# Kernel optimization log

Measured on AMD Instinct MI355X. Metric: run time of the kernel, lower is better.

Reference implementation:

```python
import jax, jax.numpy as jnp
import numpy as np

VOCAB = 8; D = 256; H = 8; DH = 32; SEQ = 4096; N_LAYERS = 4; N_CLASS = 10
BUCKET = 64; N_HASHES = 2; N_BUCKETS = SEQ // BUCKET; B = 8


def setup_inputs() -> dict:
    key = jax.random.key(0)
    ks = iter(jax.random.split(key, 24))
    s = 0.02
    inp = {}
    inp['x'] = jax.random.randint(next(ks), (B, SEQ), 0, VOCAB)
    inp['emb'] = jax.random.normal(next(ks), (VOCAB, D)) * s
    inp['posenc'] = jax.random.normal(next(ks), (SEQ, D)) * s
    inp['ln1_g'] = jnp.ones((N_LAYERS, D)); inp['ln1_b'] = jnp.zeros((N_LAYERS, D))
    inp['Wqk'] = jax.random.normal(next(ks), (N_LAYERS, D, D)) * s
    inp['Wv'] = jax.random.normal(next(ks), (N_LAYERS, D, D)) * s
    inp['Wo'] = jax.random.normal(next(ks), (N_LAYERS, D, D)) * s
    inp['ln2_g'] = jnp.ones((N_LAYERS, D)); inp['ln2_b'] = jnp.zeros((N_LAYERS, D))
    inp['W1'] = jax.random.normal(next(ks), (N_LAYERS, D, 4 * D)) * s
    inp['b1'] = jnp.zeros((N_LAYERS, 4 * D))
    inp['W2'] = jax.random.normal(next(ks), (N_LAYERS, 4 * D, D)) * s
    inp['b2'] = jnp.zeros((N_LAYERS, D))
    inp['rot'] = jax.random.normal(next(ks), (N_LAYERS, N_HASHES, DH, N_BUCKETS // 2))
    inp['Wf'] = jax.random.normal(next(ks), (SEQ * D, N_CLASS)) * s
    inp['bf'] = jnp.zeros((N_CLASS,))
    return inp


def layer_norm(x, g, b):
    m = x.mean(-1, keepdims=True)
    v = ((x - m) ** 2).mean(-1, keepdims=True)
    return (x - m) * jax.lax.rsqrt(v + 1e-5) * g + b


def look_back(t):
    # concatenate each chunk with the previous chunk (wrap-around roll, as in lucidrains)
    return jnp.concatenate([t, jnp.roll(t, 1, axis=2)], axis=3)


def lsh_attention(x, Wqk, Wv, Wo, rot):
    b, s, _ = x.shape
    qk = (x @ Wqk).reshape(b, s, H, DH).transpose(0, 2, 1, 3)  # b h s dh (shared QK)
    v = (x @ Wv).reshape(b, s, H, DH).transpose(0, 2, 1, 3)
    # LSH hashing: random rotations, bucket = argmax over [r, -r]
    r = jnp.einsum('bhsd,ndr->bhnsr', qk, rot)
    buckets = jnp.argmax(jnp.concatenate([r, -r], axis=-1), axis=-1)  # b h n s
    buckets = buckets + jnp.arange(N_HASHES)[:, None] * N_BUCKETS
    buckets = buckets.reshape(b, H, N_HASHES * s)
    ticker = jnp.arange(N_HASHES * s) % s
    sticker = jnp.argsort(buckets * s + ticker, axis=-1)  # stable sort by (bucket, pos)
    undo = jnp.argsort(sticker, axis=-1)
    st = sticker % s  # original seq positions, bucket-sorted
    sqk = jnp.take_along_axis(qk, st[..., None], axis=2)
    sv = jnp.take_along_axis(v, st[..., None], axis=2)
    nch = N_HASHES * N_BUCKETS
    bq = sqk.reshape(b, H, nch, BUCKET, DH)
    bk = bq / jnp.maximum(jnp.linalg.norm(bq, axis=-1, keepdims=True), 1e-6)  # keys = l2-normed qk
    bv = sv.reshape(b, H, nch, BUCKET, DH)
    bk, bv = look_back(bk), look_back(bv)
    stq = st.reshape(b, H, nch, BUCKET)
    stk = look_back(stq)
    dots = jnp.einsum('bhcqd,bhckd->bhcqk', bq, bk) * (DH ** -0.5)
    dots = jnp.where(stq[..., :, None] < stk[..., None, :], -1e9, dots)   # causal
    dots = jnp.where(stq[..., :, None] == stk[..., None, :], -1e5, dots)  # self-mask
    lse = jax.nn.logsumexp(dots, axis=-1, keepdims=True)
    bo = jnp.einsum('bhcqk,bhckd->bhcqd', jnp.exp(dots - lse), bv)
    so = bo.reshape(b, H, N_HASHES * s, DH)
    slog = lse.reshape(b, H, N_HASHES * s)
    o = jnp.take_along_axis(so, undo[..., None], axis=2).reshape(b, H, N_HASHES, s, DH)
    lg = jnp.take_along_axis(slog, undo, axis=2).reshape(b, H, N_HASHES, s, 1)
    out = (o * jax.nn.softmax(lg, axis=2)).sum(axis=2)  # combine hash rounds by logits
    return out.transpose(0, 2, 1, 3).reshape(b, s, D) @ Wo


def reference(x, emb, posenc, ln1_g, ln1_b, Wqk, Wv, Wo, ln2_g, ln2_b, W1, b1, W2, b2, rot, Wf, bf):
    h = emb[x] + posenc[None]
    x1, x2 = h, h  # reversible two-stream (torch.cat([x, x]))
    for l in range(N_LAYERS):
        x1 = x1 + lsh_attention(layer_norm(x2, ln1_g[l], ln1_b[l]), Wqk[l], Wv[l], Wo[l], rot[l])
        ff_in = layer_norm(x1, ln2_g[l], ln2_b[l])
        x2 = x2 + jax.nn.gelu(ff_in @ W1[l] + b1[l]) @ W2[l] + b2[l]
    y = 0.5 * (x1 + x2)  # stack(chunk(2)).mean(0)
    return y.reshape(y.shape[0], -1) @ Wf + bf
```

## Files before the change

### kernel.cpp

```cpp
#include <hip/hip_runtime.h>
#include <hip/hip_bf16.h>
#include <math.h>

#define SEQ 4096
#define D 256
#define H 8
#define DH 32
#define B 8
#define NL 4
#define NH 2
#define NTOK (B*SEQ)

__global__ __launch_bounds__(256) void k_embed(const int* __restrict__ x,
    const float* __restrict__ emb, const float* __restrict__ pos,
    float* __restrict__ x1, float* __restrict__ x2) {
  int t = blockIdx.x; int d = threadIdx.x;
  int s = t & (SEQ - 1);
  int tok = x[t];
  float v = emb[tok * D + d] + pos[(size_t)s * D + d];
  x1[(size_t)t * D + d] = v;
  x2[(size_t)t * D + d] = v;
}

__global__ __launch_bounds__(256) void k_ln(const float* __restrict__ X,
    const float* __restrict__ g, const float* __restrict__ bta,
    float* __restrict__ Y) {
  int lane = threadIdx.x & 63, wv = threadIdx.x >> 6;
  int row = blockIdx.x * 4 + wv;
  const float* xr = X + (size_t)row * D;
  float v[4]; float s = 0.f;
  #pragma unroll
  for (int j = 0; j < 4; j++) { v[j] = xr[lane + 64 * j]; s += v[j]; }
  #pragma unroll
  for (int off = 32; off; off >>= 1) s += __shfl_xor(s, off);
  float m = s * (1.0f / D);
  float vs = 0.f;
  #pragma unroll
  for (int j = 0; j < 4; j++) { float d0 = v[j] - m; vs += d0 * d0; }
  #pragma unroll
  for (int off = 32; off; off >>= 1) vs += __shfl_xor(vs, off);
  float inv = rsqrtf(vs * (1.0f / D) + 1e-5f);
  float* yr = Y + (size_t)row * D;
  #pragma unroll
  for (int j = 0; j < 4; j++) {
    int d0 = lane + 64 * j;
    yr[d0] = (v[j] - m) * inv * g[d0] + bta[d0];
  }
}

__device__ __forceinline__ float gelu_f(float x) {
  float x3 = x * x * x;
  return 0.5f * x * (1.0f + tanhf(0.7978845608028654f * (x + 0.044715f * x3)));
}

template<int MODE>
__global__ __launch_bounds__(256) void k_gemm(const float* __restrict__ A,
    const float* __restrict__ Bm, float* __restrict__ C,
    const float* __restrict__ bias, int M, int N, int K,
    int lda, int ldb, int ldc) {
  __shared__ float As[16][68];
  __shared__ float Bs[16][68];
  int tid = threadIdx.x;
  int tx = tid & 15, ty = tid >> 4;
  int row0 = blockIdx.y * 64, col0 = blockIdx.x * 64;
  int arow = tid >> 2, ac4 = tid & 3;
  int brow = tid >> 4, bc4 = tid & 15;
  float acc[4][4] = {};
  for (int k0 = 0; k0 < K; k0 += 16) {
    float4 av = *(const float4*)(A + (size_t)(row0 + arow) * lda + k0 + ac4 * 4);
    float4 bv = *(const float4*)(Bm + (size_t)(k0 + brow) * ldb + col0 + bc4 * 4);
    __syncthreads();
    As[ac4 * 4 + 0][arow] = av.x;
    As[ac4 * 4 + 1][arow] = av.y;
    As[ac4 * 4 + 2][arow] = av.z;
    As[ac4 * 4 + 3][arow] = av.w;
    *(float4*)&Bs[brow][bc4 * 4] = bv;
    __syncthreads();
    #pragma unroll
    for (int kk = 0; kk < 16; ++kk) {
      float4 a = *(float4*)&As[kk][ty * 4];
      float4 b = *(float4*)&Bs[kk][tx * 4];
      float ar[4] = {a.x, a.y, a.z, a.w};
      float br[4] = {b.x, b.y, b.z, b.w};
      #pragma unroll
      for (int i = 0; i < 4; i++)
        #pragma unroll
        for (int j = 0; j < 4; j++)
          acc[i][j] = fmaf(ar[i], br[j], acc[i][j]);
    }
  }
  #pragma unroll
  for (int i = 0; i < 4; i++) {
    int gr = row0 + ty * 4 + i;
    #pragma unroll
    for (int j = 0; j < 4; j++) {
      int gc = col0 + tx * 4 + j;
      float vv = acc[i][j];
      if constexpr (MODE == 1) {
        int b0 = gr >> 12, s0 = gr & 4095, h0 = gc >> 5, d0 = gc & 31;
        C[((size_t)(b0 * H + h0) * SEQ + s0) * DH + d0] = vv;
      } else if constexpr (MODE == 2) {
        C[(size_t)gr * ldc + gc] = gelu_f(vv + bias[gc]);
      } else {
        float add = bias ? bias[gc] : 0.f;
        C[(size_t)gr * ldc + gc] += vv + add;
      }
    }
  }
}

__global__ __launch_bounds__(256) void k_hash(const float* __restrict__ qk,
    const float* __restrict__ rot, int* __restrict__ st) {
  __shared__ float rs[32][33];
  __shared__ int sb[SEQ];
  __shared__ int hist[64];
  __shared__ int start[64];
  int tid = threadIdx.x;
  int bh = blockIdx.x >> 1, n = blockIdx.x & 1;
  const float* rotn = rot + n * DH * 32;
  for (int i = tid; i < 1024; i += 256) rs[i >> 5][i & 31] = rotn[i];
  if (tid < 64) hist[tid] = 0;
  __syncthreads();
  const float* qkb = qk + (size_t)bh * SEQ * DH;
  for (int s = tid; s < SEQ; s += 256) {
    float q[32];
    const float* qr = qkb + (size_t)s * DH;
    #pragma unroll
    for (int d = 0; d < 32; d += 4) {
      float4 t4 = *(const float4*)(qr + d);
      q[d] = t4.x; q[d + 1] = t4.y; q[d + 2] = t4.z; q[d + 3] = t4.w;
    }
    float bp = -1e30f, bn = -1e30f; int bpi = 0, bni = 0;
    for (int j = 0; j < 32; j++) {
      float rv = 0.f;
      #pragma unroll
      for (int d = 0; d < 32; d++) rv = fmaf(q[d], rs[d][j], rv);
      if (rv > bp) { bp = rv; bpi = j; }
      if (-rv > bn) { bn = -rv; bni = j; }
    }
    sb[s] = (bp >= bn) ? bpi : (bni + 32);
  }
  __syncthreads();
  for (int s = tid; s < SEQ; s += 256) atomicAdd(&hist[sb[s]], 1);
  __syncthreads();
  if (tid == 0) {
    int acc = 0;
    for (int j = 0; j < 64; j++) { start[j] = acc; acc += hist[j]; }
  }
  __syncthreads();
  if (tid < 64) {
    int j = tid;
    int* outp = st + (size_t)blockIdx.x * SEQ;
    int pos = start[j];
    for (int p = 0; p < SEQ; p++) if (sb[p] == j) outp[pos++] = p;
  }
}

template<int NHALF>
__global__ __launch_bounds__(256) void k_attn(const float* __restrict__ qk,
    const float* __restrict__ v, const int* __restrict__ st,
    float* __restrict__ o_acc, float* __restrict__ lg) {
  __shared__ float qs[64][36];
  __shared__ float vs[128][36];
  __shared__ float dots[64][129];
  __shared__ float lse_s[64];
  __shared__ int stq[64];
  __shared__ int stk[128];
  int tid = threadIdx.x;
  int bh = blockIdx.x >> 6, cl = blockIdx.x & 63;
  int c = NHALF * 64 + cl;
  int pc = (c + 127) & 127, pn = pc >> 6;
  const int* stb = st + (size_t)bh * 2 * SEQ;
  if (tid < 64) {
    int q0 = stb[NHALF * SEQ + cl * 64 + tid];
    stq[tid] = q0; stk[tid] = q0;
  } else if (tid < 128) {
    int kk = tid - 64;
    stk[64 + kk] = stb[pn * SEQ + (pc & 63) * 64 + kk];
  }
  __syncthreads();
  const float* qkb = qk + (size_t)bh * SEQ * DH;
  const float* vb  = v  + (size_t)bh * SEQ * DH;
  for (int idx = tid; idx < 512; idx += 256) {
    int r = idx >> 3, j = idx & 7;
    *(float4*)&qs[r][j * 4] = *(const float4*)(qkb + (size_t)stq[r] * DH + j * 4);
  }
  for (int idx = tid; idx < 1024; idx += 256) {
    int r = idx >> 3, j = idx & 7;
    *(float4*)&vs[r][j * 4] = *(const float4*)(vb + (size_t)stk[r] * DH + j * 4);
  }
  int col = tid & 127;
  int rh = tid >> 7;
  float4 kf[8];
  int kpos = stk[col];
  {
    const float* kr = qkb + (size_t)kpos * DH;
    float nrm = 0.f;
    #pragma unroll
    for (int j = 0; j < 8; j++) {
      kf[j] = *(const float4*)(kr + j * 4);
      nrm += kf[j].x * kf[j].x + kf[j].y * kf[j].y + kf[j].z * kf[j].z + kf[j].w * kf[j].w;
    }
    float sc = 0.17677669529663687f / fmaxf(sqrtf(nrm), 1e-6f);
    #pragma unroll
    for (int j = 0; j < 8; j++) { kf[j].x *= sc; kf[j].y *= sc; kf[j].z *= sc; kf[j].w *= sc; }
  }
  __syncthreads();
  for (int r0 = 0; r0 < 32; ++r0) {
    int r = rh * 32 + r0;
    float dsum = 0.f;
    #pragma unroll
    for (int j = 0; j < 8; j++) {
      float4 qv = *(float4*)&qs[r][j * 4];
      dsum = fmaf(qv.x, kf[j].x, dsum);
      dsum = fmaf(qv.y, kf[j].y, dsum);
      dsum = fmaf(qv.z, kf[j].z, dsum);
      dsum = fmaf(qv.w, kf[j].w, dsum);
    }
    int sq = stq[r];
    float dd = dsum;
    if (sq == kpos) dd = -1e5f;
    else if (sq < kpos) dd = -1e9f;
    dots[r][col] = dd;
  }
  __syncthreads();
  int lane = tid & 63, wv = tid >> 6;
  for (int rr = 0; rr < 16; ++rr) {
    int r = wv * 16 + rr;
    float d0 = dots[r][lane], d1 = dots[r][lane + 64];
    float m = fmaxf(d0, d1);
    #pragma unroll
    for (int off = 32; off; off >>= 1) m = fmaxf(m, __shfl_xor(m, off));
    float e0 = expf(d0 - m), e1 = expf(d1 - m);
    float ssum = e0 + e1;
    #pragma unroll
    for (int off = 32; off; off >>= 1) ssum += __shfl_xor(ssum, off);
    float inv = 1.0f / ssum;
    dots[r][lane] = e0 * inv;
    dots[r][lane + 64] = e1 * inv;
    if (lane == 0) lse_s[r] = m + logf(ssum);
  }
  __syncthreads();
  int r = tid >> 2, dq = (tid & 3) << 3;
  float4 a0 = make_float4(0, 0, 0, 0), a1 = make_float4(0, 0, 0, 0);
  for (int cc = 0; cc < 128; ++cc) {
    float p = dots[r][cc];
    float4 v0 = *(float4*)&vs[cc][dq];
    float4 v1 = *(float4*)&vs[cc][dq + 4];
    a0.x = fmaf(p, v0.x, a0.x); a0.y = fmaf(p, v0.y, a0.y);
    a0.z = fmaf(p, v0.z, a0.z); a0.w = fmaf(p, v0.w, a0.w);
    a1.x = fmaf(p, v1.x, a1.x); a1.y = fmaf(p, v1.y, a1.y);
    a1.z = fmaf(p, v1.z, a1.z); a1.w = fmaf(p, v1.w, a1.w);
  }
  int pos = stq[r];
  int b0 = bh >> 3, h0 = bh & 7;
  float* orow = o_acc + ((size_t)b0 * SEQ + pos) * D + h0 * DH + dq;
  if constexpr (NHALF == 0) {
    *(float4*)orow = a0;
    *(float4*)(orow + 4) = a1;
  } else {
    float l0 = lg[(size_t)bh * SEQ + pos];
    float l1 = lse_s[r];
    float m = fmaxf(l0, l1);
    float w0 = expf(l0 - m), w1 = expf(l1 - m);
    float inv = 1.0f / (w0 + w1);
    float4 o0 = *(float4*)orow;
    float4 o1 = *(float4*)(orow + 4);
    o0.x = (w0 * o0.x + w1 * a0.x) * inv;
    o0.y = (w0 * o0.y + w1 * a0.y) * inv;
    o0.z = (w0 * o0.z + w1 * a0.z) * inv;
    o0.w = (w0 * o0.w + w1 * a0.w) * inv;
    o1.x = (w0 * o1.x + w1 * a1.x) * inv;
    o1.y = (w0 * o1.y + w1 * a1.y) * inv;
    o1.z = (w0 * o1.z + w1 * a1.z) * inv;
    o1.w = (w0 * o1.w + w1 * a1.w) * inv;
    *(float4*)orow = o0;
    *(float4*)(orow + 4) = o1;
  }
  if constexpr (NHALF == 0) {
    if (tid < 64) lg[(size_t)bh * SEQ + stq[tid]] = lse_s[tid];
  }
}

__global__ __launch_bounds__(128) void k_initout(const float* __restrict__ bf,
                                                 float* __restrict__ outp) {
  int i = threadIdx.x;
  if (i < 80) outp[i] = bf[i % 10];
}

__global__ __launch_bounds__(256) void k_cls(const float* __restrict__ x1,
    const float* __restrict__ x2, const float* __restrict__ Wf,
    float* __restrict__ outp) {
  __shared__ float wsum[4];
  int tid = threadIdx.x;
  size_t ib = (size_t)blockIdx.x * 1024 + tid * 4;
  int lane = tid & 63, wv = tid >> 6;
  for (int b0 = 0; b0 < B; ++b0) {
    const float* p1 = x1 + (size_t)b0 * (SEQ * D) + ib;
    const float* p2 = x2 + (size_t)b0 * (SEQ * D) + ib;
    float4 y1 = *(const float4*)p1;
    float4 y2 = *(const float4*)p2;
    float y[4] = {0.5f * (y1.x + y2.x), 0.5f * (y1.y + y2.y),
                  0.5f * (y1.z + y2.z), 0.5f * (y1.w + y2.w)};
    float acc[10] = {};
    #pragma unroll
    for (int t = 0; t < 4; ++t) {
      const float* wr = Wf + (ib + t) * 10;
      #pragma unroll
      for (int c0 = 0; c0 < 10; ++c0) acc[c0] = fmaf(y[t], wr[c0], acc[c0]);
    }
    #pragma unroll 1
    for (int c0 = 0; c0 < 10; ++c0) {
      float sv = acc[c0];
      #pragma unroll
      for (int off = 32; off; off >>= 1) sv += __shfl_xor(sv, off);
      if (lane == 0) wsum[wv] = sv;
      __syncthreads();
      if (tid == 0) atomicAdd(&outp[b0 * 10 + c0], wsum[0] + wsum[1] + wsum[2] + wsum[3]);
      __syncthreads();
    }
  }
}

extern "C" void kernel_launch(void* const* d_in, const int* in_sizes, int n_in,
                              void* d_out, int out_size, void* d_ws, size_t ws_size,
                              hipStream_t stream) {
  const int*   x    = (const int*)  d_in[0];
  const float* emb  = (const float*)d_in[1];
  const float* pos  = (const float*)d_in[2];
  const float* ln1g = (const float*)d_in[3];
  const float* ln1b = (const float*)d_in[4];
  const float* Wqk  = (const float*)d_in[5];
  const float* Wv   = (const float*)d_in[6];
  const float* Wo   = (const float*)d_in[7];
  const float* ln2g = (const float*)d_in[8];
  const float* ln2b = (const float*)d_in[9];
  const float* W1   = (const float*)d_in[10];
  const float* b1   = (const float*)d_in[11];
  const float* W2   = (const float*)d_in[12];
  const float* b2   = (const float*)d_in[13];
  const float* rot  = (const float*)d_in[14];
  const float* Wf   = (const float*)d_in[15];
  const float* bf   = (const float*)d_in[16];
  float* outp = (float*)d_out;

  const size_t SZ = (size_t)NTOK * D;
  float* x1  = (float*)d_ws;
  float* x2  = x1 + SZ;
  float* tln = x1 + 2 * SZ;
  float* och = tln;
  float* qk  = x1 + 3 * SZ;
  float* vv  = x1 + 4 * SZ;
  float* lg  = x1 + 5 * SZ;
  int*   st  = (int*)(lg + (size_t)B * H * SEQ);
  float* mid = qk;

  k_embed<<<NTOK, 256, 0, stream>>>(x, emb, pos, x1, x2);
  for (int l = 0; l < NL; ++l) {
    k_ln<<<NTOK / 4, 256, 0, stream>>>(x2, ln1g + l * D, ln1b + l * D, tln);
    k_gemm<1><<<dim3(D / 64, NTOK / 64), 256, 0, stream>>>(
        tln, Wqk + (size_t)l * D * D, qk, nullptr, NTOK, D, D, D, D, 0);
    k_gemm<1><<<dim3(D / 64, NTOK / 64), 256, 0, stream>>>(
        tln, Wv + (size_t)l * D * D, vv, nullptr, NTOK, D, D, D, D, 0);
    k_hash<<<B * H * NH, 256, 0, stream>>>(qk, rot + (size_t)l * NH * DH * 32, st);
    k_attn<0><<<B * H * 64, 256, 0, stream>>>(qk, vv, st, och, lg);
    k_attn<1><<<B * H * 64, 256, 0, stream>>>(qk, vv, st, och, lg);
    k_gemm<3><<<dim3(D / 64, NTOK / 64), 256, 0, stream>>>(
        och, Wo + (size_t)l * D * D, x1, nullptr, NTOK, D, D, D, D, D);
    k_ln<<<NTOK / 4, 256, 0, stream>>>(x1, ln2g + l * D, ln2b + l * D, tln);
    k_gemm<2><<<dim3(1024 / 64, NTOK / 64), 256, 0, stream>>>(
        tln, W1 + (size_t)l * D * 1024, mid, b1 + (size_t)l * 1024,
        NTOK, 1024, D, D, 1024, 1024);
    k_gemm<3><<<dim3(D / 64, NTOK / 64), 256, 0, stream>>>(
        mid, W2 + (size_t)l * 1024 * D, x2, b2 + (size_t)l * D,
        NTOK, D, 1024, 1024, D, D);
  }
  k_initout<<<1, 128, 0, stream>>>(bf, outp);
  k_cls<<<1024, 256, 0, stream>>>(x1, x2, Wf, outp);
}
```

Measured before the change: 6.396 ms.

## Use 128x128 register-blocked FP32 GEMM with prefetch and split FFN hidden dim

The GEMM moves from 64x64 tiles with 4x4 per-thread outputs to 128x128 tiles with 8x8 per-thread outputs. Global loads for the next K-slice are prefetched into registers while the current slice is computed, and results are written as float4 vectors. The FFN is split into two 512-wide halves, with W2 accumulating into x2 after each half, so the intermediate buffer is half the size. The classifier kernel keeps Wf in registers and reduces all 10 classes together, using one sync pair per batch instead of one per class. The cost is higher register pressure, which can lower occupancy, and fewer GEMM blocks (512 for the DxD GEMMs).

```diff
diff --git a/kernel.cpp b/kernel.cpp
--- a/kernel.cpp
+++ b/kernel.cpp
@@ -10,6 +10,11 @@
 #define NL 4
 #define NH 2
 #define NTOK (B*SEQ)
+
+__device__ __forceinline__ float gelu_f(float x) {
+  float x3 = x * x * x;
+  return 0.5f * x * (1.0f + tanhf(0.7978845608028654f * (x + 0.044715f * x3)));
+}
 
 __global__ __launch_bounds__(256) void k_embed(const int* __restrict__ x,
     const float* __restrict__ emb, const float* __restrict__ pos,
@@ -48,63 +53,82 @@
   }
 }
 
-__device__ __forceinline__ float gelu_f(float x) {
-  float x3 = x * x * x;
-  return 0.5f * x * (1.0f + tanhf(0.7978845608028654f * (x + 0.044715f * x3)));
-}
-
 template<int MODE>
-__global__ __launch_bounds__(256) void k_gemm(const float* __restrict__ A,
+__global__ __launch_bounds__(256) void k_gemm_f32(const float* __restrict__ A,
     const float* __restrict__ Bm, float* __restrict__ C,
-    const float* __restrict__ bias, int M, int N, int K,
-    int lda, int ldb, int ldc) {
-  __shared__ float As[16][68];
-  __shared__ float Bs[16][68];
-  int tid = threadIdx.x;
-  int tx = tid & 15, ty = tid >> 4;
-  int row0 = blockIdx.y * 64, col0 = blockIdx.x * 64;
-  int arow = tid >> 2, ac4 = tid & 3;
-  int brow = tid >> 4, bc4 = tid & 15;
-  float acc[4][4] = {};
+    const float* __restrict__ bias, int K, int lda, int ldb, int ldc, int N) {
+  __shared__ float As[16][132];
+  __shared__ float Bs[16][132];
+  int t = threadIdx.x;
+  int tx = t & 15, ty = t >> 4;
+  int row0 = blockIdx.y * 128, col0 = blockIdx.x * 128;
+  int ar = t >> 1, akq = (t & 1) * 8;
+  int bk = t >> 4, bcq = (t & 15) * 8;
+  const float* ap = A + (size_t)(row0 + ar) * lda + akq;
+  const float* bp = Bm + (size_t)bk * ldb + col0 + bcq;
+  float4 a0 = *(const float4*)(ap);
+  float4 a1 = *(const float4*)(ap + 4);
+  float4 b0 = *(const float4*)(bp);
+  float4 b1 = *(const float4*)(bp + 4);
+  float acc[8][8] = {};
   for (int k0 = 0; k0 < K; k0 += 16) {
-    float4 av = *(const float4*)(A + (size_t)(row0 + arow) * lda + k0 + ac4 * 4);
-    float4 bv = *(const float4*)(Bm + (size_t)(k0 + brow) * ldb + col0 + bc4 * 4);
     __syncthreads();
-    As[ac4 * 4 + 0][arow] = av.x;
-    As[ac4 * 4 + 1][arow] = av.y;
-    As[ac4 * 4 + 2][arow] = av.z;
-    As[ac4 * 4 + 3][arow] = av.w;
-    *(float4*)&Bs[brow][bc4 * 4] = bv;
+    As[akq + 0][ar] = a0.x; As[akq + 1][ar] = a0.y;
+    As[akq + 2][ar] = a0.z; As[akq + 3][ar] = a0.w;
+    As[akq + 4][ar] = a1.x; As[akq + 5][ar] = a1.y;
+    As[akq + 6][ar] = a1.z; As[akq + 7][ar] = a1.w;
+    *(float4*)&Bs[bk][bcq] = b0;
+    *(float4*)&Bs[bk][bcq + 4] = b1;
     __syncthreads();
+    if (k0 + 16 < K) {
+      a0 = *(const float4*)(ap + k0 + 16);
+      a1 = *(const float4*)(ap + k0 + 20);
+      const float* bpk = Bm + (size_t)(k0 + 16 + bk) * ldb + col0 + bcq;
+      b0 = *(const float4*)(bpk);
+      b1 = *(const float4*)(bpk + 4);
+    }
     #pragma unroll
     for (int kk = 0; kk < 16; ++kk) {
-      float4 a = *(float4*)&As[kk][ty * 4];
-      float4 b = *(float4*)&Bs[kk][tx * 4];
-      float ar[4] = {a.x, a.y, a.z, a.w};
-      float br[4] = {b.x, b.y, b.z, b.w};
-      #pragma unroll
-      for (int i = 0; i < 4; i++)
+      float a[8], b[8];
+      *(float4*)&a[0] = *(float4*)&As[kk][ty * 8];
+      *(float4*)&a[4] = *(float4*)&As[kk][ty * 8 + 4];
+      *(float4*)&b[0] = *(float4*)&Bs[kk][tx * 8];
+      *(float4*)&b[4] = *(float4*)&Bs[kk][tx * 8 + 4];
+      #pragma unroll
+      for (int i = 0; i < 8; i++)
         #pragma unroll
-        for (int j = 0; j < 4; j++)
-          acc[i][j] = fmaf(ar[i], br[j], acc[i][j]);
-    }
-  }
-  #pragma unroll
-  for (int i = 0; i < 4; i++) {
-    int gr = row0 + ty * 4 + i;
-    #pragma unroll
-    for (int j = 0; j < 4; j++) {
-      int gc = col0 + tx * 4 + j;
-      float vv = acc[i][j];
-      if constexpr (MODE == 1) {
-        int b0 = gr >> 12, s0 = gr & 4095, h0 = gc >> 5, d0 = gc & 31;
-        C[((size_t)(b0 * H + h0) * SEQ + s0) * DH + d0] = vv;
-      } else if constexpr (MODE == 2) {
-        C[(size_t)gr * ldc + gc] = gelu_f(vv + bias[gc]);
-      } else {
-        float add = bias ? bias[gc] : 0.f;
-        C[(size_t)gr * ldc + gc] += vv + add;
-      }
+        for (int j = 0; j < 8; j++)
+          acc[i][j] = fmaf(a[i], b[j], acc[i][j]);
+    }
+  }
+  #pragma unroll
+  for (int i = 0; i < 8; i++) {
+    int gr = row0 + ty * 8 + i;
+    int gc0 = col0 + tx * 8;
+    if constexpr (MODE == 0) {
+      int b0i = gr >> 12, s0 = gr & 4095, h0 = gc0 >> 5, d0 = gc0 & 31;
+      float* dst = C + ((size_t)(b0i * H + h0) * SEQ + s0) * DH + d0;
+      *(float4*)dst = *(float4*)&acc[i][0];
+      *(float4*)(dst + 4) = *(float4*)&acc[i][4];
+    } else if constexpr (MODE == 2) {
+      float* dst = C + (size_t)gr * ldc + gc0;
+      float o[8];
+      #pragma unroll
+      for (int j = 0; j < 8; j++) o[j] = gelu_f(acc[i][j] + bias[gc0 + j]);
+      *(float4*)dst = *(float4*)&o[0];
+      *(float4*)(dst + 4) = *(float4*)&o[4];
+    } else {
+      float* dst = C + (size_t)gr * ldc + gc0;
+      float4 c0 = *(float4*)dst, c1 = *(float4*)(dst + 4);
+      float add[8];
+      #pragma unroll
+      for (int j = 0; j < 8; j++) add[j] = bias ? bias[gc0 + j] : 0.f;
+      c0.x += acc[i][0] + add[0]; c0.y += acc[i][1] + add[1];
+      c0.z += acc[i][2] + add[2]; c0.w += acc[i][3] + add[3];
+      c1.x += acc[i][4] + add[4]; c1.y += acc[i][5] + add[5];
+      c1.z += acc[i][6] + add[6]; c1.w += acc[i][7] + add[7];
+      *(float4*)dst = c0;
+      *(float4*)(dst + 4) = c1;
     }
   }
 }
@@ -291,34 +315,39 @@
 __global__ __launch_bounds__(256) void k_cls(const float* __restrict__ x1,
     const float* __restrict__ x2, const float* __restrict__ Wf,
     float* __restrict__ outp) {
-  __shared__ float wsum[4];
+  __shared__ float part[4][10];
   int tid = threadIdx.x;
   size_t ib = (size_t)blockIdx.x * 1024 + tid * 4;
   int lane = tid & 63, wv = tid >> 6;
+  float wf[4][10];
+  #pragma unroll
+  for (int e = 0; e < 4; e++)
+    #pragma unroll
+    for (int c = 0; c < 10; c++) wf[e][c] = Wf[(ib + e) * 10 + c];
   for (int b0 = 0; b0 < B; ++b0) {
-    const float* p1 = x1 + (size_t)b0 * (SEQ * D) + ib;
-    const float* p2 = x2 + (size_t)b0 * (SEQ * D) + ib;
-    float4 y1 = *(const float4*)p1;
-    float4 y2 = *(const float4*)p2;
+    float4 y1 = *(const float4*)(x1 + (size_t)b0 * (SEQ * D) + ib);
+    float4 y2 = *(const float4*)(x2 + (size_t)b0 * (SEQ * D) + ib);
     float y[4] = {0.5f * (y1.x + y2.x), 0.5f * (y1.y + y2.y),
                   0.5f * (y1.z + y2.z), 0.5f * (y1.w + y2.w)};
     float acc[10] = {};
     #pragma unroll
-    for (int t = 0; t < 4; ++t) {
-      const float* wr = Wf + (ib + t) * 10;
-      #pragma unroll
-      for (int c0 = 0; c0 < 10; ++c0) acc[c0] = fmaf(y[t], wr[c0], acc[c0]);
-    }
-    #pragma unroll 1
-    for (int c0 = 0; c0 < 10; ++c0) {
-      float sv = acc[c0];
-      #pragma unroll
-      for (int off = 32; off; off >>= 1) sv += __shfl_xor(sv, off);
-      if (lane == 0) wsum[wv] = sv;
-      __syncthreads();
-      if (tid == 0) atomicAdd(&outp[b0 * 10 + c0], wsum[0] + wsum[1] + wsum[2] + wsum[3]);
-      __syncthreads();
-    }
+    for (int e = 0; e < 4; e++)
+      #pragma unroll
+      for (int c = 0; c < 10; c++) acc[c] = fmaf(y[e], wf[e][c], acc[c]);
+    #pragma unroll
+    for (int c = 0; c < 10; c++) {
+      #pragma unroll
+      for (int off = 32; off; off >>= 1) acc[c] += __shfl_xor(acc[c], off);
+    }
+    if (lane == 0) {
+      #pragma unroll
+      for (int c = 0; c < 10; c++) part[wv][c] = acc[c];
+    }
+    __syncthreads();
+    if (tid < 10)
+      atomicAdd(&outp[b0 * 10 + tid],
+                part[0][tid] + part[1][tid] + part[2][tid] + part[3][tid]);
+    __syncthreads();
   }
 }
 
@@ -358,22 +387,24 @@
   k_embed<<<NTOK, 256, 0, stream>>>(x, emb, pos, x1, x2);
   for (int l = 0; l < NL; ++l) {
     k_ln<<<NTOK / 4, 256, 0, stream>>>(x2, ln1g + l * D, ln1b + l * D, tln);
-    k_gemm<1><<<dim3(D / 64, NTOK / 64), 256, 0, stream>>>(
-        tln, Wqk + (size_t)l * D * D, qk, nullptr, NTOK, D, D, D, D, 0);
-    k_gemm<1><<<dim3(D / 64, NTOK / 64), 256, 0, stream>>>(
-        tln, Wv + (size_t)l * D * D, vv, nullptr, NTOK, D, D, D, D, 0);
+    k_gemm_f32<0><<<dim3(2, 256), 256, 0, stream>>>(
+        tln, Wqk + (size_t)l * D * D, qk, nullptr, 256, 256, 256, 0, 256);
+    k_gemm_f32<0><<<dim3(2, 256), 256, 0, stream>>>(
+        tln, Wv + (size_t)l * D * D, vv, nullptr, 256, 256, 256, 0, 256);
     k_hash<<<B * H * NH, 256, 0, stream>>>(qk, rot + (size_t)l * NH * DH * 32, st);
     k_attn<0><<<B * H * 64, 256, 0, stream>>>(qk, vv, st, och, lg);
     k_attn<1><<<B * H * 64, 256, 0, stream>>>(qk, vv, st, och, lg);
-    k_gemm<3><<<dim3(D / 64, NTOK / 64), 256, 0, stream>>>(
-        och, Wo + (size_t)l * D * D, x1, nullptr, NTOK, D, D, D, D, D);
+    k_gemm_f32<3><<<dim3(2, 256), 256, 0, stream>>>(
+        och, Wo + (size_t)l * D * D, x1, nullptr, 256, 256, 256, 256, 256);
     k_ln<<<NTOK / 4, 256, 0, stream>>>(x1, ln2g + l * D, ln2b + l * D, tln);
-    k_gemm<2><<<dim3(1024 / 64, NTOK / 64), 256, 0, stream>>>(
-        tln, W1 + (size_t)l * D * 1024, mid, b1 + (size_t)l * 1024,
-        NTOK, 1024, D, D, 1024, 1024);
-    k_gemm<3><<<dim3(D / 64, NTOK / 64), 256, 0, stream>>>(
-        mid, W2 + (size_t)l * 1024 * D, x2, b2 + (size_t)l * D,
-        NTOK, D, 1024, 1024, D, D);
+    for (int h = 0; h < 2; ++h) {
+      k_gemm_f32<2><<<dim3(4, 256), 256, 0, stream>>>(
+          tln, W1 + (size_t)l * D * 1024 + h * 512, mid,
+          b1 + (size_t)l * 1024 + h * 512, 256, 256, 1024, 512, 512);
+      k_gemm_f32<3><<<dim3(2, 256), 256, 0, stream>>>(
+          mid, W2 + (size_t)l * 1024 * D + (size_t)h * 512 * D, x2,
+          h == 0 ? b2 + (size_t)l * D : nullptr, 512, 512, 256, 256, 256);
+    }
   }
   k_initout<<<1, 128, 0, stream>>>(bf, outp);
   k_cls<<<1024, 256, 0, stream>>>(x1, x2, Wf, outp);
```

After: 5.779 ms. 9.7% less time.
